# Optimization experiments

Hardware: AMD Instinct MI355X
Metric: run time of the kernel (lower is better)

Reference implementation:

```python
import jax, jax.numpy as jnp
import numpy as np

N, E, H, P = 50000, 300000, 128, 3
NODE_IN, EDGE_IN, OUT = 15, 7, 3


def _ln(x, g, b, eps=1e-5):
    m = jnp.mean(x, axis=-1, keepdims=True)
    v = jnp.mean((x - m) ** 2, axis=-1, keepdims=True)
    return (x - m) * jax.lax.rsqrt(v + eps) * g + b


def _mlp(x, w1, b1, w2, b2):
    # Linear -> ReLU -> Linear (matches MLP(hidden_dims=(H,)))
    return jnp.maximum(x @ w1 + b1, 0.0) @ w2 + b2


def setup_inputs() -> dict:
    key = jax.random.key(0)
    ks = iter(jax.random.split(key, 64))

    def nrm(shape, s=0.05):
        return jax.random.normal(next(ks), shape, dtype=jnp.float32) * s

    inp = {}
    inp['x'] = nrm((N, NODE_IN), 1.0)
    inp['e'] = nrm((E, EDGE_IN), 1.0)
    inp['edge_index'] = jax.random.randint(next(ks), (2, E), 0, N, dtype=jnp.int32)
    # node encoder
    inp['enc_n_w1'] = nrm((NODE_IN, H)); inp['enc_n_b1'] = jnp.zeros((H,), jnp.float32)
    inp['enc_n_w2'] = nrm((H, H)); inp['enc_n_b2'] = jnp.zeros((H,), jnp.float32)
    inp['enc_n_g'] = jnp.ones((H,), jnp.float32); inp['enc_n_be'] = jnp.zeros((H,), jnp.float32)
    # edge encoder
    inp['enc_e_w1'] = nrm((EDGE_IN, H)); inp['enc_e_b1'] = jnp.zeros((H,), jnp.float32)
    inp['enc_e_w2'] = nrm((H, H)); inp['enc_e_b2'] = jnp.zeros((H,), jnp.float32)
    inp['enc_e_g'] = jnp.ones((H,), jnp.float32); inp['enc_e_be'] = jnp.zeros((H,), jnp.float32)
    # per-processor edge MLP (in = 3H) and node MLP (in = 2H), stacked over P steps
    inp['pe_w1'] = nrm((P, 3 * H, H)); inp['pe_b1'] = jnp.zeros((P, H), jnp.float32)
    inp['pe_w2'] = nrm((P, H, H)); inp['pe_b2'] = jnp.zeros((P, H), jnp.float32)
    inp['pe_g'] = jnp.ones((P, H), jnp.float32); inp['pe_be'] = jnp.zeros((P, H), jnp.float32)
    inp['pn_w1'] = nrm((P, 2 * H, H)); inp['pn_b1'] = jnp.zeros((P, H), jnp.float32)
    inp['pn_w2'] = nrm((P, H, H)); inp['pn_b2'] = jnp.zeros((P, H), jnp.float32)
    inp['pn_g'] = jnp.ones((P, H), jnp.float32); inp['pn_be'] = jnp.zeros((P, H), jnp.float32)
    # node decoder (no layer norm)
    inp['dec_w1'] = nrm((H, H)); inp['dec_b1'] = jnp.zeros((H,), jnp.float32)
    inp['dec_w2'] = nrm((H, OUT)); inp['dec_b2'] = jnp.zeros((OUT,), jnp.float32)
    return inp


def _forward(edge_index, x, e,
             enc_n_w1, enc_n_b1, enc_n_w2, enc_n_b2, enc_n_g, enc_n_be,
             enc_e_w1, enc_e_b1, enc_e_w2, enc_e_b2, enc_e_g, enc_e_be,
             pe_w1, pe_b1, pe_w2, pe_b2, pe_g, pe_be,
             pn_w1, pn_b1, pn_w2, pn_b2, pn_g, pn_be,
             dec_w1, dec_b1, dec_w2, dec_b2):
    row, col = edge_index[0], edge_index[1]  # PyG: x_j = x[row] (source), x_i = x[col] (target)
    xh = _ln(_mlp(x, enc_n_w1, enc_n_b1, enc_n_w2, enc_n_b2), enc_n_g, enc_n_be)
    eh = _ln(_mlp(e, enc_e_w1, enc_e_b1, enc_e_w2, enc_e_b2), enc_e_g, enc_e_be)
    for i in range(P):
        # message: edge_mlp(cat[x_i, x_j, edge_attr]) -> scatter-add onto targets (col)
        msg = _ln(_mlp(jnp.concatenate([xh[col], xh[row], eh], axis=-1),
                       pe_w1[i], pe_b1[i], pe_w2[i], pe_b2[i]), pe_g[i], pe_be[i])
        aggr = jax.ops.segment_sum(msg, col, num_segments=N)  # [N, H]
        new_x = _ln(_mlp(jnp.concatenate([aggr, xh], axis=-1),
                         pn_w1[i], pn_b1[i], pn_w2[i], pn_b2[i]), pn_g[i], pn_be[i]) + xh
        # edge update uses cat[x[row], x[col], e] (note: order differs from message)
        new_e = _ln(_mlp(jnp.concatenate([xh[row], xh[col], eh], axis=-1),
                         pe_w1[i], pe_b1[i], pe_w2[i], pe_b2[i]), pe_g[i], pe_be[i]) + eh
        xh, eh = new_x, new_e
    return jnp.maximum(xh @ dec_w1 + dec_b1, 0.0) @ dec_w2 + dec_b2


def reference(x, e, edge_index,
              enc_n_w1, enc_n_b1, enc_n_w2, enc_n_b2, enc_n_g, enc_n_be,
              enc_e_w1, enc_e_b1, enc_e_w2, enc_e_b2, enc_e_g, enc_e_be,
              pe_w1, pe_b1, pe_w2, pe_b2, pe_g, pe_be,
              pn_w1, pn_b1, pn_w2, pn_b2, pn_g, pn_be,
              dec_w1, dec_b1, dec_w2, dec_b2):
    return _forward(edge_index, x, e,
                    enc_n_w1, enc_n_b1, enc_n_w2, enc_n_b2, enc_n_g, enc_n_be,
                    enc_e_w1, enc_e_b1, enc_e_w2, enc_e_b2, enc_e_g, enc_e_be,
                    pe_w1, pe_b1, pe_w2, pe_b2, pe_g, pe_be,
                    pn_w1, pn_b1, pn_w2, pn_b2, pn_g, pn_be,
                    dec_w1, dec_b1, dec_w2, dec_b2)
```

## Files before the change

### kernel.cpp

```cpp
#include <hip/hip_runtime.h>
#include <stdint.h>
#include <math.h>

#define DEVI __device__ __forceinline__

typedef __attribute__((ext_vector_type(8))) _Float16 f16x8;
typedef __attribute__((ext_vector_type(4))) float f32x4;

#define LO_SCALE 2048.0f
#define LO_INV (1.0f / 2048.0f)
#define LO_INV_D (1.0 / 2048.0)
#define AGG_SCALE_D 4194304.0
#define AGG_INV_D (1.0 / 4194304.0)

DEVI unsigned short f2h(float f) {
  union { _Float16 h; unsigned short u; } v; v.h = (_Float16)f; return v.u;
}
DEVI float h2f(unsigned short u) {
  union { unsigned short u; _Float16 h; } v; v.u = u; return (float)v.h;
}
DEVI unsigned short loPart(float v, unsigned short hi) {
  return f2h((v - h2f(hi)) * LO_SCALE);
}
DEVI f32x4 mfma16(f16x8 a, f16x8 b, f32x4 c) {
  return __builtin_amdgcn_mfma_f32_16x16x32_f16(a, b, c, 0, 0, 0);
}
DEVI void mfma4(f16x8 ah, f16x8 al, f16x8 bh, f16x8 bl,
                f32x4& acc, f32x4& accx, f32x4& accy) {
  acc  = mfma16(ah, bh, acc);
  accx = mfma16(ah, bl, accx);
  accx = mfma16(al, bh, accx);
  accy = mfma16(al, bl, accy);
}
DEVI float combine3(float a, float ax, float ay, float b) {
  return (float)((double)a + ((double)ax + (double)ay * LO_INV_D) * LO_INV_D + (double)b);
}
DEVI int swz(int row, int col) { return row * 128 + (col ^ ((row & 7) << 3)); }

struct KParams {
  const unsigned short* w1h; const unsigned short* w1l;
  const unsigned short* w2h; const unsigned short* w2l;
  const float* b1; const float* b2; const float* g; const float* be;
  const float* srcA;
  const unsigned short* xhi;
  const unsigned short* xlo;
  float* xf;
  float* ef;
  unsigned short* xhi_out; unsigned short* xlo_out;
  const int* rowi; const int* coli;
  int* aggi;
  float* out;
  const float* w2f; const float* b2f;
  int nrows; int kin;
};

struct RepackItem { const float* src; unsigned short* dst; int K; int Kt; };
struct RepackParams { RepackItem it[17]; };

__global__ __launch_bounds__(256) void repack_kernel(RepackParams rp) {
  const RepackItem w = rp.it[blockIdx.y];
  const int f = blockIdx.x;
  if (f >= w.Kt * 8) return;
  const int kt = f >> 3, nt = f & 7;
  const size_t loOff = (size_t)w.Kt * 8 * 512;
  for (int s = threadIdx.x; s < 512; s += 256) {
    int ln = s >> 3, j = s & 7;
    int k = kt * 32 + ((ln >> 4) << 3) + j;
    int c = nt * 16 + (ln & 15);
    float v = (k < w.K) ? w.src[(size_t)k * 128 + c] : 0.f;
    unsigned short hi = f2h(v);
    w.dst[(size_t)f * 512 + s] = hi;
    w.dst[loOff + (size_t)f * 512 + s] = loPart(v, hi);
  }
}

template <int MODE>
__global__ __launch_bounds__((MODE == 2) ? 768 : 256, (MODE == 2) ? 1 : 2)
void gnn_kernel(KParams p) {
  constexpr int NT = (MODE == 2) ? 768 : 256;
  constexpr int REG = (MODE == 2) ? 12288 : 8192;
  constexpr int NREG = (MODE == 2 || MODE == 3) ? 2 : 1;
  __shared__ __align__(16) unsigned short stA[NREG * 2 * REG];
  __shared__ __align__(16) unsigned short wbuf[(MODE == 2) ? 16384 : 1];
  __shared__ float w2s[(MODE == 4) ? 392 : 1];

  const int tid = threadIdx.x;
  const int lane = tid & 63;
  const int wave = tid >> 6;
  const int w4 = (MODE == 2) ? (wave % 6) : wave;
  const int vrt = (MODE == 2) ? (wave / 6) : 0;
  const int r0 = blockIdx.x * ((MODE == 2) ? 96 : 64);
  const int l15 = lane & 15;
  const int lg = lane >> 4;

  auto HI = [&](int t) { return stA + 2 * t * REG; };
  auto LO = [&](int t) { return stA + 2 * t * REG + REG; };

  auto stageW = [&](int s, int buf) {
    const unsigned short* h = (s < 12) ? p.w1h + s * 4096 : p.w2h + (s - 12) * 4096;
    const unsigned short* l = (s < 12) ? p.w1l + s * 4096 : p.w2l + (s - 12) * 4096;
    for (int i = tid; i < 1024; i += NT) {
      *(f16x8*)&wbuf[buf * 8192 + i * 8] =
          *(const f16x8*)((i < 512) ? h + i * 8 : l + (i - 512) * 8);
    }
  };

  if constexpr (MODE == 3) {
    for (int s = tid; s < 1024; s += NT) {
      int row = s >> 4, cc = (s & 15) * 8;
      int n = r0 + row;
      int off = swz(row, cc);
      if (n < p.nrows) {
        const int* ap = p.aggi + (size_t)n * 128 + cc;
        union { unsigned short u[8]; f16x8 v; } th, tl;
#pragma unroll
        for (int j = 0; j < 8; j++) {
          float v = (float)((double)ap[j] * AGG_INV_D);
          th.u[j] = f2h(v); tl.u[j] = loPart(v, th.u[j]);
        }
        *(f16x8*)&HI(0)[off] = th.v; *(f16x8*)&LO(0)[off] = tl.v;
        *(f16x8*)&HI(1)[off] = *(const f16x8*)(p.xhi + (size_t)n * 128 + cc);
        *(f16x8*)&LO(1)[off] = *(const f16x8*)(p.xlo + (size_t)n * 128 + cc);
      } else {
        f16x8 z = {0,0,0,0,0,0,0,0};
        *(f16x8*)&HI(0)[off] = z; *(f16x8*)&LO(0)[off] = z;
        *(f16x8*)&HI(1)[off] = z; *(f16x8*)&LO(1)[off] = z;
      }
    }
  } else if constexpr (MODE == 0 || MODE == 1) {
    for (int s = tid; s < 256; s += NT) {
      int row = s >> 2, cc = (s & 3) * 8;
      int n = r0 + row;
      union { unsigned short u[8]; f16x8 v; } th, tl;
#pragma unroll
      for (int j = 0; j < 8; j++) {
        int k = cc + j;
        float v = (n < p.nrows && k < p.kin) ? p.srcA[(size_t)n * p.kin + k] : 0.f;
        th.u[j] = f2h(v); tl.u[j] = loPart(v, th.u[j]);
      }
      int off = swz(row, cc);
      *(f16x8*)&HI(0)[off] = th.v; *(f16x8*)&LO(0)[off] = tl.v;
    }
  } else if constexpr (MODE == 4) {
    for (int s = tid; s < 1024; s += NT) {
      int row = s >> 4, cc = (s & 15) * 8;
      int n = r0 + row;
      int off = swz(row, cc);
      f16x8 z = {0,0,0,0,0,0,0,0};
      if (n < p.nrows) {
        *(f16x8*)&HI(0)[off] = *(const f16x8*)(p.xhi + (size_t)n * 128 + cc);
        *(f16x8*)&LO(0)[off] = *(const f16x8*)(p.xlo + (size_t)n * 128 + cc);
      } else { *(f16x8*)&HI(0)[off] = z; *(f16x8*)&LO(0)[off] = z; }
    }
    for (int s = tid; s < 387; s += NT) w2s[s] = (s < 384) ? p.w2f[s] : p.b2f[s - 384];
  } else {
    stageW(0, 0);
  }
  __syncthreads();

  constexpr int K1T = (MODE == 2) ? 12 : (MODE == 3) ? 8 : (MODE == 4) ? 4 : 1;
  const f32x4 zz = {0.f, 0.f, 0.f, 0.f};
  f32x4 acc1[8], acc1x[8], acc1y[8];
#pragma unroll
  for (int nt = 0; nt < 8; nt++) { acc1[nt] = zz; acc1x[nt] = zz; acc1y[nt] = zz; }
  const int arow = w4 * 16 + l15;
  const int acol = lg << 3;

  if constexpr (MODE == 2) {
    const int ridx = r0 + arow;
    const int ec = (ridx < p.nrows) ? ridx : 0;
    const int nc = p.coli[ec], nr = p.rowi[ec];
    const unsigned short* aH = p.xhi + (size_t)(vrt ? nr : nc) * 128;
    const unsigned short* aL = p.xlo + (size_t)(vrt ? nr : nc) * 128;
    const unsigned short* bH = p.xhi + (size_t)(vrt ? nc : nr) * 128;
    const unsigned short* bL = p.xlo + (size_t)(vrt ? nc : nr) * 128;
    const float* ep = p.ef + (size_t)ec * 128;
#pragma unroll
    for (int kt = 0; kt < 12; kt++) {
      const int cur = kt & 1;
      const int nxt = cur ^ 1;
      stageW(kt + 1, nxt);
      const int kc = (kt & 3) * 32 + acol;
      f16x8 ah, al;
      if (kt < 4)      { ah = *(const f16x8*)(aH + kc); al = *(const f16x8*)(aL + kc); }
      else if (kt < 8) { ah = *(const f16x8*)(bH + kc); al = *(const f16x8*)(bL + kc); }
      else {
        union { unsigned short u[8]; f16x8 v; } th, tl;
#pragma unroll
        for (int j = 0; j < 8; j++) {
          float v = ep[kc + j];
          th.u[j] = f2h(v); tl.u[j] = loPart(v, th.u[j]);
        }
        ah = th.v; al = tl.v;
      }
#pragma unroll
      for (int nt = 0; nt < 8; nt++) {
        f16x8 bh = *(const f16x8*)&wbuf[cur * 8192 + nt * 512 + lane * 8];
        f16x8 bl = *(const f16x8*)&wbuf[cur * 8192 + 4096 + nt * 512 + lane * 8];
        mfma4(ah, al, bh, bl, acc1[nt], acc1x[nt], acc1y[nt]);
      }
      __syncthreads();
    }
  } else {
#pragma unroll
    for (int kt = 0; kt < K1T; kt++) {
      int t = kt >> 2;
      int so = swz(arow, (kt & 3) * 32 + acol);
      f16x8 ah = *(const f16x8*)&HI(t)[so];
      f16x8 al = *(const f16x8*)&LO(t)[so];
#pragma unroll
      for (int nt = 0; nt < 8; nt++) {
        f16x8 bh = *(const f16x8*)&p.w1h[(size_t)(kt * 8 + nt) * 512 + lane * 8];
        f16x8 bl = *(const f16x8*)&p.w1l[(size_t)(kt * 8 + nt) * 512 + lane * 8];
        mfma4(ah, al, bh, bl, acc1[nt], acc1x[nt], acc1y[nt]);
      }
    }
  }

  float b1c[8];
#pragma unroll
  for (int nt = 0; nt < 8; nt++) b1c[nt] = p.b1[nt * 16 + l15];
#pragma unroll
  for (int nt = 0; nt < 8; nt++) {
#pragma unroll
    for (int r = 0; r < 4; r++) {
      int row = w4 * 16 + (lg << 2) + r;
      int col = nt * 16 + l15;
      int off = swz(row, col);
      float v = combine3(acc1[nt][r], acc1x[nt][r], acc1y[nt][r], b1c[nt]);
      v = v > 0.f ? v : 0.f;
      unsigned short hi = f2h(v);
      HI(vrt)[off] = hi; LO(vrt)[off] = loPart(v, hi);
    }
  }

  if constexpr (MODE != 4) {
    f32x4 acc2[8], acc2x[8], acc2y[8];
#pragma unroll
    for (int nt = 0; nt < 8; nt++) { acc2[nt] = zz; acc2x[nt] = zz; acc2y[nt] = zz; }
#pragma unroll
    for (int kt = 0; kt < 4; kt++) {
      if constexpr (MODE == 2) {
        const int cur = (12 + kt) & 1;
        if (kt < 3) stageW(13 + kt, cur ^ 1);
        int so = swz(arow, kt * 32 + acol);
        f16x8 ah = *(const f16x8*)&HI(vrt)[so];
        f16x8 al = *(const f16x8*)&LO(vrt)[so];
#pragma unroll
        for (int nt = 0; nt < 8; nt++) {
          f16x8 bh = *(const f16x8*)&wbuf[cur * 8192 + nt * 512 + lane * 8];
          f16x8 bl = *(const f16x8*)&wbuf[cur * 8192 + 4096 + nt * 512 + lane * 8];
          mfma4(ah, al, bh, bl, acc2[nt], acc2x[nt], acc2y[nt]);
        }
        if (kt < 3) __syncthreads();
      } else {
        int so = swz(arow, kt * 32 + acol);
        f16x8 ah = *(const f16x8*)&HI(vrt)[so];
        f16x8 al = *(const f16x8*)&LO(vrt)[so];
#pragma unroll
        for (int nt = 0; nt < 8; nt++) {
          f16x8 bh = *(const f16x8*)&p.w2h[(size_t)(kt * 8 + nt) * 512 + lane * 8];
          f16x8 bl = *(const f16x8*)&p.w2l[(size_t)(kt * 8 + nt) * 512 + lane * 8];
          mfma4(ah, al, bh, bl, acc2[nt], acc2x[nt], acc2y[nt]);
        }
      }
    }

    float b2c[8], gc[8], bec[8];
#pragma unroll
    for (int nt = 0; nt < 8; nt++) {
      int c = nt * 16 + l15;
      b2c[nt] = p.b2[c]; gc[nt] = p.g[c]; bec[nt] = p.be[c];
    }
    {
      double sum[4] = {0.0, 0.0, 0.0, 0.0};
#pragma unroll
      for (int nt = 0; nt < 8; nt++)
#pragma unroll
        for (int r = 0; r < 4; r++) {
          acc2[nt][r] = combine3(acc2[nt][r], acc2x[nt][r], acc2y[nt][r], b2c[nt]);
          sum[r] += (double)acc2[nt][r];
        }
#pragma unroll
      for (int r = 0; r < 4; r++) {
#pragma unroll
        for (int m = 1; m < 16; m <<= 1) sum[r] += __shfl_xor(sum[r], m);
        sum[r] *= (1.0 / 128.0);
      }
      double vs[4] = {0.0, 0.0, 0.0, 0.0};
#pragma unroll
      for (int nt = 0; nt < 8; nt++)
#pragma unroll
        for (int r = 0; r < 4; r++) {
          double d = (double)acc2[nt][r] - sum[r];
          vs[r] += d * d;
        }
#pragma unroll
      for (int r = 0; r < 4; r++) {
#pragma unroll
        for (int m = 1; m < 16; m <<= 1) vs[r] += __shfl_xor(vs[r], m);
        vs[r] = 1.0 / sqrt(vs[r] * (1.0 / 128.0) + 1e-5);
      }
#pragma unroll
      for (int nt = 0; nt < 8; nt++)
#pragma unroll
        for (int r = 0; r < 4; r++)
          acc2[nt][r] = (float)(((double)acc2[nt][r] - sum[r]) * vs[r]) * gc[nt] + bec[nt];
    }

    if constexpr (MODE == 2) __syncthreads();

#pragma unroll
    for (int r = 0; r < 4; r++) {
      int idx = r0 + w4 * 16 + (lg << 2) + r;
      if (idx >= p.nrows) continue;
      if constexpr (MODE == 0) {
        float* xr = p.xf + (size_t)idx * 128;
        unsigned short* xh_ = p.xhi_out + (size_t)idx * 128;
        unsigned short* xl_ = p.xlo_out + (size_t)idx * 128;
#pragma unroll
        for (int nt = 0; nt < 8; nt++) {
          int c = nt * 16 + l15; float v = acc2[nt][r];
          xr[c] = v;
          unsigned short hi = f2h(v);
          xh_[c] = hi; xl_[c] = loPart(v, hi);
        }
      } else if constexpr (MODE == 1) {
        float* er = p.ef + (size_t)idx * 128;
#pragma unroll
        for (int nt = 0; nt < 8; nt++) er[nt * 16 + l15] = acc2[nt][r];
      } else if constexpr (MODE == 3) {
        float* xr = p.xf + (size_t)idx * 128;
        unsigned short* xh_ = p.xhi_out + (size_t)idx * 128;
        unsigned short* xl_ = p.xlo_out + (size_t)idx * 128;
#pragma unroll
        for (int nt = 0; nt < 8; nt++) {
          int c = nt * 16 + l15;
          float v = acc2[nt][r] + xr[c];
          xr[c] = v;
          unsigned short hi = f2h(v);
          xh_[c] = hi; xl_[c] = loPart(v, hi);
        }
      } else {
        if (vrt == 0) {
          int tgt = p.coli[idx];
          int* ar = p.aggi + (size_t)tgt * 128;
#pragma unroll
          for (int nt = 0; nt < 8; nt++) {
            int q = __double2int_rn((double)acc2[nt][r] * AGG_SCALE_D);
            atomicAdd(&ar[nt * 16 + l15], q);
          }
        } else {
          float* er = p.ef + (size_t)idx * 128;
#pragma unroll
          for (int nt = 0; nt < 8; nt++) {
            int c = nt * 16 + l15;
            er[c] = acc2[nt][r] + er[c];
          }
        }
      }
    }
  } else {
    __syncthreads();
    if (tid < 192) {
      int row = tid / 3, oc = tid - row * 3;
      int n = r0 + row;
      if (n < p.nrows) {
        double s = (double)w2s[384 + oc];
        for (int k = 0; k < 128; k++) {
          int off = swz(row, k);
          double h = (double)h2f(HI(0)[off]) + (double)h2f(LO(0)[off]) * LO_INV_D;
          s += h * (double)w2s[k * 3 + oc];
        }
        p.out[(size_t)n * 3 + oc] = (float)s;
      }
    }
  }
}

extern "C" void kernel_launch(void* const* d_in, const int* in_sizes, int n_in,
                              void* d_out, int out_size, void* d_ws, size_t ws_size,
                              hipStream_t stream) {
  if (n_in < 31) return;
  const int N = in_sizes[0] / 15;
  const int E = in_sizes[1] / 7;
  const float* x        = (const float*)d_in[0];
  const float* ein      = (const float*)d_in[1];
  const int*   eidx     = (const int*)d_in[2];
  const float* enc_n_w1 = (const float*)d_in[3];
  const float* enc_n_b1 = (const float*)d_in[4];
  const float* enc_n_w2 = (const float*)d_in[5];
  const float* enc_n_b2 = (const float*)d_in[6];
  const float* enc_n_g  = (const float*)d_in[7];
  const float* enc_n_be = (const float*)d_in[8];
  const float* enc_e_w1 = (const float*)d_in[9];
  const float* enc_e_b1 = (const float*)d_in[10];
  const float* enc_e_w2 = (const float*)d_in[11];
  const float* enc_e_b2 = (const float*)d_in[12];
  const float* enc_e_g  = (const float*)d_in[13];
  const float* enc_e_be = (const float*)d_in[14];
  const float* pe_w1    = (const float*)d_in[15];
  const float* pe_b1    = (const float*)d_in[16];
  const float* pe_w2    = (const float*)d_in[17];
  const float* pe_b2    = (const float*)d_in[18];
  const float* pe_g     = (const float*)d_in[19];
  const float* pe_be    = (const float*)d_in[20];
  const float* pn_w1    = (const float*)d_in[21];
  const float* pn_b1    = (const float*)d_in[22];
  const float* pn_w2    = (const float*)d_in[23];
  const float* pn_b2    = (const float*)d_in[24];
  const float* pn_g     = (const float*)d_in[25];
  const float* pn_be    = (const float*)d_in[26];
  const float* dec_w1   = (const float*)d_in[27];
  const float* dec_b1   = (const float*)d_in[28];
  const float* dec_w2   = (const float*)d_in[29];
  const float* dec_b2   = (const float*)d_in[30];

  char* ws = (char*)d_ws;
  size_t off = 0;
  auto carve = [&](size_t bytes) -> void* {
    void* pp = ws + off; off += (bytes + 255) & ~(size_t)255; return pp;
  };
  float* xh            = (float*)carve((size_t)N * 128 * 4);
  unsigned short* xhi  = (unsigned short*)carve((size_t)N * 128 * 2);
  unsigned short* xlo  = (unsigned short*)carve((size_t)N * 128 * 2);
  float* eh            = (float*)carve((size_t)E * 128 * 4);
  int* aggi            = (int*)carve((size_t)N * 128 * 4);

  const int ktab[17] = {15, 128, 7, 128, 384, 384, 384, 128, 128, 128,
                        256, 256, 256, 128, 128, 128, 128};
  unsigned short* pk[17];
  for (int i = 0; i < 17; i++) {
    int kt = (ktab[i] + 31) / 32;
    pk[i] = (unsigned short*)carve((size_t)2 * kt * 8 * 512 * 2);
  }
  if (off > ws_size) return;

  RepackParams rp;
  const float* wsrc[17] = {enc_n_w1, enc_n_w2, enc_e_w1, enc_e_w2,
                           pe_w1, pe_w1 + 384 * 128, pe_w1 + 2 * 384 * 128,
                           pe_w2, pe_w2 + 128 * 128, pe_w2 + 2 * 128 * 128,
                           pn_w1, pn_w1 + 256 * 128, pn_w1 + 2 * 256 * 128,
                           pn_w2, pn_w2 + 128 * 128, pn_w2 + 2 * 128 * 128,
                           dec_w1};
  for (int i = 0; i < 17; i++) {
    rp.it[i].src = wsrc[i]; rp.it[i].dst = pk[i];
    rp.it[i].K = ktab[i]; rp.it[i].Kt = (ktab[i] + 31) / 32;
  }
  repack_kernel<<<dim3(96, 17), 256, 0, stream>>>(rp);

  auto wlo = [&](int i) { return pk[i] + (size_t)((ktab[i] + 31) / 32) * 8 * 512; };
  const int gN = (N + 63) / 64, gE = (E + 63) / 64, gE96 = (E + 95) / 96;

  {
    KParams kp{};
    kp.w1h = pk[0]; kp.w1l = wlo(0); kp.w2h = pk[1]; kp.w2l = wlo(1);
    kp.b1 = enc_n_b1; kp.b2 = enc_n_b2; kp.g = enc_n_g; kp.be = enc_n_be;
    kp.srcA = x; kp.xf = xh; kp.xhi_out = xhi; kp.xlo_out = xlo;
    kp.nrows = N; kp.kin = 15;
    gnn_kernel<0><<<gN, 256, 0, stream>>>(kp);
  }
  {
    KParams kp{};
    kp.w1h = pk[2]; kp.w1l = wlo(2); kp.w2h = pk[3]; kp.w2l = wlo(3);
    kp.b1 = enc_e_b1; kp.b2 = enc_e_b2; kp.g = enc_e_g; kp.be = enc_e_be;
    kp.srcA = ein; kp.ef = eh; kp.nrows = E; kp.kin = 7;
    gnn_kernel<1><<<gE, 256, 0, stream>>>(kp);
  }
  for (int i = 0; i < 3; i++) {
    hipMemsetAsync(aggi, 0, (size_t)N * 128 * 4, stream);
    {
      KParams kp{};
      kp.w1h = pk[4 + i]; kp.w1l = wlo(4 + i);
      kp.w2h = pk[7 + i]; kp.w2l = wlo(7 + i);
      kp.b1 = pe_b1 + i * 128; kp.b2 = pe_b2 + i * 128;
      kp.g = pe_g + i * 128; kp.be = pe_be + i * 128;
      kp.xhi = xhi; kp.xlo = xlo; kp.ef = eh;
      kp.rowi = eidx; kp.coli = eidx + E;
      kp.aggi = aggi; kp.nrows = E;
      gnn_kernel<2><<<gE96, 768, 0, stream>>>(kp);
    }
    {
      KParams kp{};
      kp.w1h = pk[10 + i]; kp.w1l = wlo(10 + i);
      kp.w2h = pk[13 + i]; kp.w2l = wlo(13 + i);
      kp.b1 = pn_b1 + i * 128; kp.b2 = pn_b2 + i * 128;
      kp.g = pn_g + i * 128; kp.be = pn_be + i * 128;
      kp.aggi = aggi; kp.xhi = xhi; kp.xlo = xlo;
      kp.xf = xh; kp.xhi_out = xhi; kp.xlo_out = xlo; kp.nrows = N;
      gnn_kernel<3><<<gN, 256, 0, stream>>>(kp);
    }
  }
  {
    KParams kp{};
    kp.w1h = pk[16]; kp.w1l = wlo(16); kp.b1 = dec_b1;
    kp.xhi = xhi; kp.xlo = xlo; kp.w2f = dec_w2; kp.b2f = dec_b2;
    kp.out = (float*)d_out; kp.nrows = N;
    gnn_kernel<4><<<gN, 256, 0, stream>>>(kp);
  }
}
```

Measured before the change: 1.892 ms.

## Split edge-kernel output columns across wave pairs with cross-wave LayerNorm reduction

The edge processor kernel now runs 1024 threads per block over 64 edges instead of 768 threads over 96 edges. Each pair of waves splits the 128 output columns into two halves of 4 tiles each, which halves the accumulator registers per wave. LayerNorm statistics are combined across the pair through a shared-memory double buffer, which adds extra barriers. The aim is to cut register pressure and raise wave-level parallelism, at the cost of more synchronisation and more blocks.

```diff
diff --git a/kernel.cpp b/kernel.cpp
--- a/kernel.cpp
+++ b/kernel.cpp
@@ -75,21 +75,25 @@
 }
 
 template <int MODE>
-__global__ __launch_bounds__((MODE == 2) ? 768 : 256, (MODE == 2) ? 1 : 2)
+__global__ __launch_bounds__((MODE == 2) ? 1024 : 256, (MODE == 2) ? 1 : 2)
 void gnn_kernel(KParams p) {
-  constexpr int NT = (MODE == 2) ? 768 : 256;
-  constexpr int REG = (MODE == 2) ? 12288 : 8192;
+  constexpr int NT = (MODE == 2) ? 1024 : 256;
+  constexpr int REG = 8192;
   constexpr int NREG = (MODE == 2 || MODE == 3) ? 2 : 1;
+  constexpr int NTL = (MODE == 2) ? 4 : 8;
   __shared__ __align__(16) unsigned short stA[NREG * 2 * REG];
   __shared__ __align__(16) unsigned short wbuf[(MODE == 2) ? 16384 : 1];
+  __shared__ double lnbuf[(MODE == 2) ? 512 : 1];
   __shared__ float w2s[(MODE == 4) ? 392 : 1];
 
   const int tid = threadIdx.x;
   const int lane = tid & 63;
   const int wave = tid >> 6;
-  const int w4 = (MODE == 2) ? (wave % 6) : wave;
-  const int vrt = (MODE == 2) ? (wave / 6) : 0;
-  const int r0 = blockIdx.x * ((MODE == 2) ? 96 : 64);
+  const int w4 = (MODE == 2) ? ((wave >> 1) & 3) : wave;
+  const int vrt = (MODE == 2) ? (wave >> 3) : 0;
+  const int ntg = (MODE == 2) ? (wave & 1) : 0;
+  const int cb = ntg * 4;
+  const int r0 = blockIdx.x * 64;
   const int l15 = lane & 15;
   const int lg = lane >> 4;
 
@@ -160,9 +164,9 @@
 
   constexpr int K1T = (MODE == 2) ? 12 : (MODE == 3) ? 8 : (MODE == 4) ? 4 : 1;
   const f32x4 zz = {0.f, 0.f, 0.f, 0.f};
-  f32x4 acc1[8], acc1x[8], acc1y[8];
-#pragma unroll
-  for (int nt = 0; nt < 8; nt++) { acc1[nt] = zz; acc1x[nt] = zz; acc1y[nt] = zz; }
+  f32x4 acc1[NTL], acc1x[NTL], acc1y[NTL];
+#pragma unroll
+  for (int nt = 0; nt < NTL; nt++) { acc1[nt] = zz; acc1x[nt] = zz; acc1y[nt] = zz; }
   const int arow = w4 * 16 + l15;
   const int acol = lg << 3;
 
@@ -178,8 +182,7 @@
 #pragma unroll
     for (int kt = 0; kt < 12; kt++) {
       const int cur = kt & 1;
-      const int nxt = cur ^ 1;
-      stageW(kt + 1, nxt);
+      stageW(kt + 1, cur ^ 1);
       const int kc = (kt & 3) * 32 + acol;
       f16x8 ah, al;
       if (kt < 4)      { ah = *(const f16x8*)(aH + kc); al = *(const f16x8*)(aL + kc); }
@@ -194,9 +197,9 @@
         ah = th.v; al = tl.v;
       }
 #pragma unroll
-      for (int nt = 0; nt < 8; nt++) {
-        f16x8 bh = *(const f16x8*)&wbuf[cur * 8192 + nt * 512 + lane * 8];
-        f16x8 bl = *(const f16x8*)&wbuf[cur * 8192 + 4096 + nt * 512 + lane * 8];
+      for (int nt = 0; nt < NTL; nt++) {
+        f16x8 bh = *(const f16x8*)&wbuf[cur * 8192 + (cb + nt) * 512 + lane * 8];
+        f16x8 bl = *(const f16x8*)&wbuf[cur * 8192 + 4096 + (cb + nt) * 512 + lane * 8];
         mfma4(ah, al, bh, bl, acc1[nt], acc1x[nt], acc1y[nt]);
       }
       __syncthreads();
@@ -209,7 +212,7 @@
       f16x8 ah = *(const f16x8*)&HI(t)[so];
       f16x8 al = *(const f16x8*)&LO(t)[so];
 #pragma unroll
-      for (int nt = 0; nt < 8; nt++) {
+      for (int nt = 0; nt < NTL; nt++) {
         f16x8 bh = *(const f16x8*)&p.w1h[(size_t)(kt * 8 + nt) * 512 + lane * 8];
         f16x8 bl = *(const f16x8*)&p.w1l[(size_t)(kt * 8 + nt) * 512 + lane * 8];
         mfma4(ah, al, bh, bl, acc1[nt], acc1x[nt], acc1y[nt]);
@@ -217,15 +220,15 @@
     }
   }
 
-  float b1c[8];
-#pragma unroll
-  for (int nt = 0; nt < 8; nt++) b1c[nt] = p.b1[nt * 16 + l15];
-#pragma unroll
-  for (int nt = 0; nt < 8; nt++) {
+  float b1c[NTL];
+#pragma unroll
+  for (int nt = 0; nt < NTL; nt++) b1c[nt] = p.b1[(cb + nt) * 16 + l15];
+#pragma unroll
+  for (int nt = 0; nt < NTL; nt++) {
 #pragma unroll
     for (int r = 0; r < 4; r++) {
       int row = w4 * 16 + (lg << 2) + r;
-      int col = nt * 16 + l15;
+      int col = (cb + nt) * 16 + l15;
       int off = swz(row, col);
       float v = combine3(acc1[nt][r], acc1x[nt][r], acc1y[nt][r], b1c[nt]);
       v = v > 0.f ? v : 0.f;
@@ -233,11 +236,12 @@
       HI(vrt)[off] = hi; LO(vrt)[off] = loPart(v, hi);
     }
   }
+  if constexpr (MODE == 2) __syncthreads();
 
   if constexpr (MODE != 4) {
-    f32x4 acc2[8], acc2x[8], acc2y[8];
-#pragma unroll
-    for (int nt = 0; nt < 8; nt++) { acc2[nt] = zz; acc2x[nt] = zz; acc2y[nt] = zz; }
+    f32x4 acc2[NTL], acc2x[NTL], acc2y[NTL];
+#pragma unroll
+    for (int nt = 0; nt < NTL; nt++) { acc2[nt] = zz; acc2x[nt] = zz; acc2y[nt] = zz; }
 #pragma unroll
     for (int kt = 0; kt < 4; kt++) {
       if constexpr (MODE == 2) {
@@ -247,9 +251,9 @@
         f16x8 ah = *(const f16x8*)&HI(vrt)[so];
         f16x8 al = *(const f16x8*)&LO(vrt)[so];
 #pragma unroll
-        for (int nt = 0; nt < 8; nt++) {
-          f16x8 bh = *(const f16x8*)&wbuf[cur * 8192 + nt * 512 + lane * 8];
-          f16x8 bl = *(const f16x8*)&wbuf[cur * 8192 + 4096 + nt * 512 + lane * 8];
+        for (int nt = 0; nt < NTL; nt++) {
+          f16x8 bh = *(const f16x8*)&wbuf[cur * 8192 + (cb + nt) * 512 + lane * 8];
+          f16x8 bl = *(const f16x8*)&wbuf[cur * 8192 + 4096 + (cb + nt) * 512 + lane * 8];
           mfma4(ah, al, bh, bl, acc2[nt], acc2x[nt], acc2y[nt]);
         }
         if (kt < 3) __syncthreads();
@@ -258,7 +262,7 @@
         f16x8 ah = *(const f16x8*)&HI(vrt)[so];
         f16x8 al = *(const f16x8*)&LO(vrt)[so];
 #pragma unroll
-        for (int nt = 0; nt < 8; nt++) {
+        for (int nt = 0; nt < NTL; nt++) {
           f16x8 bh = *(const f16x8*)&p.w2h[(size_t)(kt * 8 + nt) * 512 + lane * 8];
           f16x8 bl = *(const f16x8*)&p.w2l[(size_t)(kt * 8 + nt) * 512 + lane * 8];
           mfma4(ah, al, bh, bl, acc2[nt], acc2x[nt], acc2y[nt]);
@@ -266,16 +270,67 @@
       }
     }
 
-    float b2c[8], gc[8], bec[8];
-#pragma unroll
-    for (int nt = 0; nt < 8; nt++) {
-      int c = nt * 16 + l15;
+    float b2c[NTL], gc[NTL], bec[NTL];
+#pragma unroll
+    for (int nt = 0; nt < NTL; nt++) {
+      int c = (cb + nt) * 16 + l15;
       b2c[nt] = p.b2[c]; gc[nt] = p.g[c]; bec[nt] = p.be[c];
     }
-    {
+    if constexpr (MODE == 2) {
+      const int slot = ((vrt * 4 + w4) * 4 + lg) * 4;
+      double ps[4] = {0.0, 0.0, 0.0, 0.0};
+#pragma unroll
+      for (int nt = 0; nt < NTL; nt++)
+#pragma unroll
+        for (int r = 0; r < 4; r++) {
+          acc2[nt][r] = combine3(acc2[nt][r], acc2x[nt][r], acc2y[nt][r], b2c[nt]);
+          ps[r] += (double)acc2[nt][r];
+        }
+#pragma unroll
+      for (int r = 0; r < 4; r++)
+#pragma unroll
+        for (int m = 1; m < 16; m <<= 1) ps[r] += __shfl_xor(ps[r], m);
+      if (l15 == 0) {
+#pragma unroll
+        for (int r = 0; r < 4; r++) lnbuf[(slot + r) * 2 + ntg] = ps[r];
+      }
+      __syncthreads();
+      double mean[4];
+#pragma unroll
+      for (int r = 0; r < 4; r++)
+        mean[r] = (lnbuf[(slot + r) * 2] + lnbuf[(slot + r) * 2 + 1]) * (1.0 / 128.0);
+      double pv[4] = {0.0, 0.0, 0.0, 0.0};
+#pragma unroll
+      for (int nt = 0; nt < NTL; nt++)
+#pragma unroll
+        for (int r = 0; r < 4; r++) {
+          double d = (double)acc2[nt][r] - mean[r];
+          pv[r] += d * d;
+        }
+#pragma unroll
+      for (int r = 0; r < 4; r++)
+#pragma unroll
+        for (int m = 1; m < 16; m <<= 1) pv[r] += __shfl_xor(pv[r], m);
+      if (l15 == 0) {
+#pragma unroll
+        for (int r = 0; r < 4; r++) lnbuf[256 + (slot + r) * 2 + ntg] = pv[r];
+      }
+      __syncthreads();
+      double rs[4];
+#pragma unroll
+      for (int r = 0; r < 4; r++) {
+        double var = lnbuf[256 + (slot + r) * 2] + lnbuf[256 + (slot + r) * 2 + 1];
+        rs[r] = 1.0 / sqrt(var * (1.0 / 128.0) + 1e-5);
+      }
+#pragma unroll
+      for (int nt = 0; nt < NTL; nt++)
+#pragma unroll
+        for (int r = 0; r < 4; r++)
+          acc2[nt][r] = (float)(((double)acc2[nt][r] - mean[r]) * rs[r]) * gc[nt] + bec[nt];
+    } else {
       double sum[4] = {0.0, 0.0, 0.0, 0.0};
 #pragma unroll
-      for (int nt = 0; nt < 8; nt++)
+      for (int nt = 0; nt < NTL; nt++)
 #pragma unroll
         for (int r = 0; r < 4; r++) {
           acc2[nt][r] = combine3(acc2[nt][r], acc2x[nt][r], acc2y[nt][r], b2c[nt]);
@@ -289,7 +344,7 @@
       }
       double vs[4] = {0.0, 0.0, 0.0, 0.0};
 #pragma unroll
-      for (int nt = 0; nt < 8; nt++)
+      for (int nt = 0; nt < NTL; nt++)
 #pragma unroll
         for (int r = 0; r < 4; r++) {
           double d = (double)acc2[nt][r] - sum[r];
@@ -302,7 +357,7 @@
         vs[r] = 1.0 / sqrt(vs[r] * (1.0 / 128.0) + 1e-5);
       }
 #pragma unroll
-      for (int nt = 0; nt < 8; nt++)
+      for (int nt = 0; nt < NTL; nt++)
 #pragma unroll
         for (int r = 0; r < 4; r++)
           acc2[nt][r] = (float)(((double)acc2[nt][r] - sum[r]) * vs[r]) * gc[nt] + bec[nt];
@@ -319,8 +374,8 @@
         unsigned short* xh_ = p.xhi_out + (size_t)idx * 128;
         unsigned short* xl_ = p.xlo_out + (size_t)idx * 128;
 #pragma unroll
-        for (int nt = 0; nt < 8; nt++) {
-          int c = nt * 16 + l15; float v = acc2[nt][r];
+        for (int nt = 0; nt < NTL; nt++) {
+          int c = (cb + nt) * 16 + l15; float v = acc2[nt][r];
           xr[c] = v;
           unsigned short hi = f2h(v);
           xh_[c] = hi; xl_[c] = loPart(v, hi);
@@ -328,14 +383,14 @@
       } else if constexpr (MODE == 1) {
         float* er = p.ef + (size_t)idx * 128;
 #pragma unroll
-        for (int nt = 0; nt < 8; nt++) er[nt * 16 + l15] = acc2[nt][r];
+        for (int nt = 0; nt < NTL; nt++) er[(cb + nt) * 16 + l15] = acc2[nt][r];
       } else if constexpr (MODE == 3) {
         float* xr = p.xf + (size_t)idx * 128;
         unsigned short* xh_ = p.xhi_out + (size_t)idx * 128;
         unsigned short* xl_ = p.xlo_out + (size_t)idx * 128;
 #pragma unroll
-        for (int nt = 0; nt < 8; nt++) {
-          int c = nt * 16 + l15;
+        for (int nt = 0; nt < NTL; nt++) {
+          int c = (cb + nt) * 16 + l15;
           float v = acc2[nt][r] + xr[c];
           xr[c] = v;
           unsigned short hi = f2h(v);
@@ -346,15 +401,15 @@
           int tgt = p.coli[idx];
           int* ar = p.aggi + (size_t)tgt * 128;
 #pragma unroll
-          for (int nt = 0; nt < 8; nt++) {
+          for (int nt = 0; nt < NTL; nt++) {
             int q = __double2int_rn((double)acc2[nt][r] * AGG_SCALE_D);
-            atomicAdd(&ar[nt * 16 + l15], q);
+            atomicAdd(&ar[(cb + nt) * 16 + l15], q);
           }
         } else {
           float* er = p.ef + (size_t)idx * 128;
 #pragma unroll
-          for (int nt = 0; nt < 8; nt++) {
-            int c = nt * 16 + l15;
+          for (int nt = 0; nt < NTL; nt++) {
+            int c = (cb + nt) * 16 + l15;
             er[c] = acc2[nt][r] + er[c];
           }
         }
@@ -450,7 +505,7 @@
   repack_kernel<<<dim3(96, 17), 256, 0, stream>>>(rp);
 
   auto wlo = [&](int i) { return pk[i] + (size_t)((ktab[i] + 31) / 32) * 8 * 512; };
-  const int gN = (N + 63) / 64, gE = (E + 63) / 64, gE96 = (E + 95) / 96;
+  const int gN = (N + 63) / 64, gE = (E + 63) / 64;
 
   {
     KParams kp{};
@@ -478,7 +533,7 @@
       kp.xhi = xhi; kp.xlo = xlo; kp.ef = eh;
       kp.rowi = eidx; kp.coli = eidx + E;
       kp.aggi = aggi; kp.nrows = E;
-      gnn_kernel<2><<<gE96, 768, 0, stream>>>(kp);
+      gnn_kernel<2><<<gE, 1024, 0, stream>>>(kp);
     }
     {
       KParams kp{};
```

Measured after the change: 2.168 ms. +14.6%, slower.
